# Kernel optimization log

Measured on AMD Instinct MI355X. Metric: run time of the kernel, lower is better.

## Reference

```python
import jax, jax.numpy as jnp
import numpy as np

ORDER = 2  # gcn_order (max diffusion step)


def _diffusion_conv(x, supports, W, b):
    """DCRNN diffusion graph conv.
    x: (B, C, N); supports: list of (N, N); W: (C*(len(supports)*ORDER+1), O); b: (O,)
    Chebyshev-style recurrence x_k = 2*A@x_{k-1} - x_{k-2}, as in original DCRNN.
    """
    feats = [x]
    for A in supports:
        x0 = x
        x1 = jnp.einsum('bcn,mn->bcm', x0, A)
        feats.append(x1)
        for _ in range(2, ORDER + 1):
            x2 = 2.0 * jnp.einsum('bcn,mn->bcm', x1, A) - x0
            feats.append(x2)
            x0, x1 = x1, x2
    h = jnp.concatenate(feats, axis=1)  # (B, C*num_matrices, N)
    return jnp.einsum('bcn,co->bon', h, W) + b[None, :, None]


def setup_inputs() -> dict:
    key = jax.random.key(0)
    ks = jax.random.split(key, 8)
    B, IN_DIM, HID, N = 64, 2, 64, 2048
    NUM_MAT = 2 * ORDER + 1  # num_supports*order + 1
    CIN = IN_DIM + HID  # 66
    inputs = jax.random.normal(ks[0], (B, IN_DIM, N), dtype=jnp.float32)
    hx = jax.random.normal(ks[1], (B, HID, N), dtype=jnp.float32)
    # random-walk style supports: nonnegative, row-normalized
    a0 = jax.random.uniform(ks[2], (N, N), dtype=jnp.float32)
    a1 = jax.random.uniform(ks[3], (N, N), dtype=jnp.float32)
    support0 = a0 / jnp.sum(a0, axis=1, keepdims=True)
    support1 = a1 / jnp.sum(a1, axis=1, keepdims=True)
    scale = 1.0 / np.sqrt(CIN * NUM_MAT)
    W_ru = jax.random.normal(ks[4], (CIN * NUM_MAT, 2 * HID), dtype=jnp.float32) * scale
    b_ru = jnp.ones((2 * HID,), dtype=jnp.float32)  # bias_start = 1.0
    W_c = jax.random.normal(ks[5], (CIN * NUM_MAT, HID), dtype=jnp.float32) * scale
    b_c = jnp.zeros((HID,), dtype=jnp.float32)
    return {"inputs": inputs, "hx": hx, "support0": support0, "support1": support1,
            "W_ru": W_ru, "b_ru": b_ru, "W_c": W_c, "b_c": b_c}


def reference(inputs, hx, support0, support1, W_ru, b_ru, W_c, b_c):
    supports = [support0, support1]
    hid = hx.shape[1]
    concat_input = jnp.concatenate([inputs, hx], axis=1)  # (B, in+hid, N)
    value = jax.nn.sigmoid(_diffusion_conv(concat_input, supports, W_ru, b_ru))
    r = value[:, :hid, :]
    u = value[:, hid:, :]
    C = jnp.tanh(_diffusion_conv(jnp.concatenate([inputs, r * hx], axis=1), supports, W_c, b_c))
    new_state = u * hx + (1.0 - u) * C
    return new_state
```

## Files before the change

### kernel.cpp

```cpp
#include <hip/hip_runtime.h>
#include <stdint.h>


typedef unsigned short ushort_t;
typedef __attribute__((ext_vector_type(8))) __bf16 bf16x8;
typedef __attribute__((ext_vector_type(4))) float f32x4;
typedef __attribute__((ext_vector_type(16))) float f32x16;
typedef __attribute__((ext_vector_type(8))) int i32x8;

#define KP 352
#define MROWS 131072

__device__ __forceinline__ ushort_t f2bf(float f) {
  union { float f; uint32_t u; } v; v.f = f;
  uint32_t r = v.u + 0x7FFFu + ((v.u >> 16) & 1u);
  return (ushort_t)(r >> 16);
}
__device__ __forceinline__ float bf2f(ushort_t u) {
  union { uint32_t u; float f; } v; v.u = ((uint32_t)u) << 16;
  return v.f;
}

__device__ __forceinline__ void gl_lds16(const void* g, void* l) {
  __builtin_amdgcn_global_load_lds(
      (const __attribute__((address_space(1))) void*)g,
      (__attribute__((address_space(3))) void*)l, 16, 0, 0);
}


__global__ void k_cast_f8(const float* __restrict__ src, uint32_t* __restrict__ dst,
                          int n4, float scale) {
  for (int i = blockIdx.x * 256 + threadIdx.x; i < n4; i += gridDim.x * 256) {
    float4 v = ((const float4*)src)[i];
    int r = __builtin_amdgcn_cvt_pk_fp8_f32(v.x * scale, v.y * scale, 0, 0);
    r = __builtin_amdgcn_cvt_pk_fp8_f32(v.z * scale, v.w * scale, r, 1);
    dst[i] = (uint32_t)r;
  }
}

__global__ void k_build_X(const float* __restrict__ inputs, const float* __restrict__ hx,
                          ushort_t* __restrict__ Xbf, uint8_t* __restrict__ Xf8) {
  int r = blockIdx.x;
  int b = r / 66, c = r - b * 66;
  const float* src = (c < 2) ? (inputs + ((size_t)b * 2 + c) * 2048)
                             : (hx + ((size_t)b * 64 + (c - 2)) * 2048);
  ushort_t* d1 = Xbf + (size_t)r * 2048;
  uint8_t* d2 = Xf8 + (size_t)r * 2048;
  for (int n = threadIdx.x * 4; n < 2048; n += 256 * 4) {
    float4 v = *(const float4*)(src + n);
    ushort4 rr;
    rr.x = f2bf(v.x); rr.y = f2bf(v.y); rr.z = f2bf(v.z); rr.w = f2bf(v.w);
    *(ushort4*)(d1 + n) = rr;
    int r8 = __builtin_amdgcn_cvt_pk_fp8_f32(v.x, v.y, 0, 0);
    r8 = __builtin_amdgcn_cvt_pk_fp8_f32(v.z, v.w, r8, 1);
    *(uint32_t*)(d2 + n) = (uint32_t)r8;
  }
}

__global__ void k_pack_W(const float* __restrict__ Wru, const float* __restrict__ Wc,
                         ushort_t* __restrict__ Wtru, ushort_t* __restrict__ Wtc) {
  int o = blockIdx.x;
  const float* W = (o < 128) ? Wru : Wc;
  int O = (o < 128) ? 128 : 64;
  int oo = (o < 128) ? o : (o - 128);
  ushort_t* Wt = (o < 128) ? Wtru : Wtc;
  for (int k = threadIdx.x; k < KP; k += 256) {
    float v = (k < 330 && oo < O) ? W[(size_t)k * O + oo] : 0.f;
    Wt[(size_t)oo * KP + k] = f2bf(v);
  }
}

__global__ __launch_bounds__(256) void k_trans_slot0(const ushort_t* __restrict__ Xbf,
                                                     ushort_t* __restrict__ Ht) {
  __shared__ ushort_t t[66 * 136];
  const int tid = threadIdx.x;
  const int b = blockIdx.y;
  const int n0 = blockIdx.x * 128;
  for (int idx = tid; idx < 66 * 16; idx += 256) {
    int c = idx >> 4, seg = idx & 15;
    bf16x8 v = *(const bf16x8*)&Xbf[((size_t)b * 66 + c) * 2048 + n0 + seg * 8];
    *(bf16x8*)&t[c * 136 + seg * 8] = v;
  }
  __syncthreads();
  for (int idx = tid; idx < 128 * 33; idx += 256) {
    int nn = idx / 33, pc = idx - nn * 33;
    int c = pc * 2;
    uint32_t pk = (uint32_t)t[c * 136 + nn] | ((uint32_t)t[(c + 1) * 136 + nn] << 16);
    *(uint32_t*)&Ht[((size_t)b * 2048 + n0 + nn) * KP + c] = pk;
  }
}

template <int MODE>
__global__ __launch_bounds__(256, 4) void gemm_bt(
    const uint8_t* __restrict__ Aop, int lda,
    const uint8_t* __restrict__ Bop,
    const ushort_t* __restrict__ Xres,
    uint8_t* __restrict__ Y1f8,
    ushort_t* __restrict__ Ht) {
  __shared__ char smem[33280];
  ushort_t* smemU = (ushort_t*)smem;
  const int tid = threadIdx.x;
  const int l = tid & 63, w = tid >> 6;
  const int wr = w >> 1, wc = w & 1;
  const int rowL = l & 31;
  const int kh = l >> 5;
  const int m7 = (rowL >> 2) & 7;

  const int fid = blockIdx.y * 33 + blockIdx.x;
  const int xcd = fid & 7;
  const int idx = fid >> 3;
  const int nb = xcd * 4 + idx / 33;
  const int mb = idx % 33;
  const int r0 = mb * 128;
  const int m0 = nb * 128;
  const int g = m0 >> 11;
  if (MODE == 1) Aop += (size_t)g * 2048;

  const int SA = (MODE == 0) ? 0x7F7F7F7F : 0x7A7A7A7A;
  const int SB = 0x76767676;

  f32x16 acc[2][2];
#pragma unroll
  for (int mi = 0; mi < 2; ++mi)
#pragma unroll
    for (int ni = 0; ni < 2; ++ni)
#pragma unroll
      for (int q = 0; q < 16; ++q) acc[mi][ni][q] = 0.f;

  const int d = tid;
  const int srow = ((d >> 3) << 2) | (((d >> 1) ^ (d >> 4)) & 1) |
                   ((((d >> 2) ^ (d >> 5)) & 1) << 1);
  const int sj = (d ^ (d >> 3)) & 1;
  const uint8_t* pA = Aop + (size_t)(r0 + srow) * lda + sj * 16;
  const uint8_t* pB = Bop + (size_t)(m0 + srow) * 2048 + sj * 16;

  const int sj0 = ((rowL * 2) ^ m7) * 16;
  const int sj1 = ((rowL * 2 + 1) ^ m7) * 16;
  const int aw = wr * 2048;
  const int bw = wc * 2048;

  const int kt0 = (idx & 3) * 4;
  for (int ktt = 0; ktt < 16; ++ktt) {
    const int kt = (ktt + kt0) & 15;
    const int kb = kt * 128;
#pragma unroll
    for (int kq = 0; kq < 4; ++kq) {
      gl_lds16(pA + kb + kq * 32, smem + kq * 4096 + tid * 16);
      gl_lds16(pB + kb + kq * 32, smem + 16384 + kq * 4096 + tid * 16);
    }
    __syncthreads();
#pragma unroll
    for (int kw = 0; kw < 2; ++kw) {
      const int rbase = (2 * kw + kh) * 4096;
      union { uint4 q[2]; i32x8 v; } bu[2], au;
#pragma unroll
      for (int ni = 0; ni < 2; ++ni) {
        const char* bp = smem + 16384 + rbase + bw + ni * 1024;
        bu[ni].q[0] = *(const uint4*)(bp + sj0);
        bu[ni].q[1] = *(const uint4*)(bp + sj1);
      }
#pragma unroll
      for (int mi = 0; mi < 2; ++mi) {
        const char* ap = smem + rbase + aw + mi * 1024;
        au.q[0] = *(const uint4*)(ap + sj0);
        au.q[1] = *(const uint4*)(ap + sj1);
#pragma unroll
        for (int ni = 0; ni < 2; ++ni)
          acc[mi][ni] = __builtin_amdgcn_mfma_scale_f32_32x32x64_f8f6f4(
              au.v, bu[ni].v, acc[mi][ni], 0, 0, 0, SA, 0, SB);
      }
    }
    __syncthreads();
  }

#pragma unroll
  for (int mi = 0; mi < 2; ++mi) {
#pragma unroll
    for (int ni = 0; ni < 2; ++ni) {
      const int clb = wc * 64 + ni * 32 + rowL;
#pragma unroll
      for (int q = 0; q < 16; ++q) {
        const int rl = wr * 64 + mi * 32 + (q & 3) + 8 * (q >> 2) + 4 * kh;
        float v = acc[mi][ni][q];
        if (MODE == 1)
          v = 2.f * v - bf2f(Xres[(size_t)(r0 + rl) * 2048 + ((m0 + clb) & 2047)]);
        smemU[clb * 130 + rl] = f2bf(v);
      }
    }
  }
  __syncthreads();

  const int slotBase = (MODE == 0 ? 1 : 2) + 2 * g;
  const int n_base = m0 & 2047;
#pragma unroll 4
  for (int j2 = 0; j2 < 32; ++j2) {
    int idx2 = j2 * 256 + tid;
    int mc = idx2 >> 6, pr = idx2 & 63;
    int rl = pr * 2;
    unsigned rg = (unsigned)(r0 + rl);
    unsigned b = rg / 66u;
    unsigned c = rg - b * 66u;
    int n = n_base + mc;
    uint32_t pk = (uint32_t)smemU[mc * 130 + rl] |
                  ((uint32_t)smemU[mc * 130 + rl + 1] << 16);
    *(uint32_t*)&Ht[((size_t)b * 2048 + n) * KP + slotBase * 66 + c] = pk;
  }

  if (MODE == 0) {
#pragma unroll 4
    for (int it = 0; it < 16; ++it) {
      int idx2 = it * 256 + tid;
      int rl = idx2 >> 5, mq = idx2 & 31;
      float v0 = bf2f(smemU[(mq * 4 + 0) * 130 + rl]) * 32.f;
      float v1 = bf2f(smemU[(mq * 4 + 1) * 130 + rl]) * 32.f;
      float v2 = bf2f(smemU[(mq * 4 + 2) * 130 + rl]) * 32.f;
      float v3 = bf2f(smemU[(mq * 4 + 3) * 130 + rl]) * 32.f;
      int r8 = __builtin_amdgcn_cvt_pk_fp8_f32(v0, v1, 0, 0);
      r8 = __builtin_amdgcn_cvt_pk_fp8_f32(v2, v3, r8, 1);
      *(uint32_t*)(Y1f8 + (size_t)(r0 + rl) * 4096 + m0 + mq * 4) = (uint32_t)r8;
    }
  }
}

template <int MODE>
__global__ __launch_bounds__(256, 4) void proj_mfma(
    const ushort_t* __restrict__ Ht_c, const ushort_t* __restrict__ Wt,
    const float* __restrict__ bias, const float* __restrict__ hx,
    ushort_t* __restrict__ Xbf, uint8_t* __restrict__ Xf8,
    ushort_t* __restrict__ Ubuf, ushort_t* __restrict__ HtW,
    float* __restrict__ out) {
  __shared__ ushort_t smem[16640];
  const int tid = threadIdx.x;
  const int l = tid & 63, w = tid >> 6;
  const int wr = w >> 1, wc = w & 1;
  const int lr = l & 15, lk = l >> 4;
  const int bb = blockIdx.x >> 4;
  const int n0 = (blockIdx.x & 15) * 128;
  const size_t m0 = (size_t)bb * 2048 + n0;

  f32x4 acc[4][4];
  const f32x4 zero = {0.f, 0.f, 0.f, 0.f};
#pragma unroll
  for (int mi = 0; mi < 4; mi++)
#pragma unroll
    for (int ni = 0; ni < 4; ni++) acc[mi][ni] = zero;

  const int srow = tid >> 2;
  const int kcol = ((tid & 3) ^ ((tid >> 3) & 3)) * 8;
  const ushort_t* pA = Ht_c + (m0 + srow) * KP + kcol;
  const ushort_t* pB = Wt + (size_t)srow * KP + kcol;
  const int so = (lk ^ ((lr >> 1) & 3)) * 8;

#define STAGEP(KT, BB)                                                         \
  {                                                                            \
    const int kp_ = (KT) * 32;                                                 \
    gl_lds16(pA + kp_, (void*)&smem[(BB) + tid * 8]);                          \
    gl_lds16(pA + (size_t)64 * KP + kp_, (void*)&smem[(BB) + 2048 + tid * 8]); \
    gl_lds16(pB + kp_, (void*)&smem[(BB) + 4096 + tid * 8]);                   \
    gl_lds16(pB + (size_t)64 * KP + kp_, (void*)&smem[(BB) + 6144 + tid * 8]); \
  }

#define COMPUTEP(BB)                                                           \
  {                                                                            \
    bf16x8 af[4], bfv[4];                                                      \
    _Pragma("unroll")                                                          \
    for (int i = 0; i < 4; i++)                                                \
      af[i] = *(const bf16x8*)&smem[(BB) + (wr * 64 + i * 16 + lr) * 32 + so]; \
    _Pragma("unroll")                                                          \
    for (int i = 0; i < 4; i++)                                                \
      bfv[i] = *(const bf16x8*)&smem[(BB) + 4096 + (wc * 64 + i * 16 + lr) * 32 + so]; \
    _Pragma("unroll")                                                          \
    for (int mi = 0; mi < 4; mi++)                                             \
      _Pragma("unroll")                                                        \
      for (int ni = 0; ni < 4; ni++)                                           \
        acc[mi][ni] = __builtin_amdgcn_mfma_f32_16x16x32_bf16(af[mi], bfv[ni], \
                                                              acc[mi][ni], 0, 0, 0); \
  }

  STAGEP(0, 0);
  __syncthreads();
#pragma unroll 1
  for (int kt = 0; kt < 11; ++kt) {
    if (kt + 1 < 11) STAGEP(kt + 1, ((kt + 1) & 1) * 8192);
    COMPUTEP((kt & 1) * 8192);
    __syncthreads();
  }

#undef STAGEP
#undef COMPUTEP

#pragma unroll
  for (int mi = 0; mi < 4; mi++) {
#pragma unroll
    for (int ni = 0; ni < 4; ni++) {
      const int rl0 = wr * 64 + mi * 16 + lk * 4;
      const int o = wc * 64 + ni * 16 + lr;
      float bv = (MODE == 0 || o < 64) ? bias[o] : 0.f;
#pragma unroll
      for (int j = 0; j < 4; j++) {
        float v = acc[mi][ni][j] + bv;
        float s;
        if (MODE == 0) s = 1.f / (1.f + expf(-v));
        else           s = tanhf(v);
        smem[o * 130 + rl0 + j] = f2bf(s);
      }
    }
  }
  __syncthreads();

  if (MODE == 0) {
#pragma unroll 4
    for (int j2 = 0; j2 < 64; ++j2) {
      int idx = j2 * 256 + tid;
      int o = idx >> 7, m = idx & 127;
      ushort_t sv = smem[o * 130 + m];
      if (o < 64) {
        float p = bf2f(sv) * hx[((size_t)bb * 64 + o) * 2048 + n0 + m];
        smem[o * 130 + m] = f2bf(p);
      } else {
        Ubuf[((size_t)bb * 64 + (o - 64)) * 2048 + n0 + m] = sv;
      }
    }
    __syncthreads();
#pragma unroll 2
    for (int j2 = 0; j2 < 8; ++j2) {
      int idx = j2 * 256 + tid;
      int o = idx >> 5, m4 = (idx & 31) * 4;
      ushort_t s0 = smem[o * 130 + m4 + 0], s1 = smem[o * 130 + m4 + 1];
      ushort_t s2 = smem[o * 130 + m4 + 2], s3 = smem[o * 130 + m4 + 3];
      ushort4 pk4; pk4.x = s0; pk4.y = s1; pk4.z = s2; pk4.w = s3;
      *(ushort4*)&Xbf[((size_t)bb * 66 + 2 + o) * 2048 + n0 + m4] = pk4;
      int r8 = __builtin_amdgcn_cvt_pk_fp8_f32(bf2f(s0), bf2f(s1), 0, 0);
      r8 = __builtin_amdgcn_cvt_pk_fp8_f32(bf2f(s2), bf2f(s3), r8, 1);
      *(uint32_t*)(Xf8 + ((size_t)bb * 66 + 2 + o) * 2048 + n0 + m4) = (uint32_t)r8;
    }
#pragma unroll 2
    for (int j2 = 0; j2 < 16; ++j2) {
      int idx = j2 * 256 + tid;
      int m = idx >> 5, po = idx & 31;
      int o = po * 2;
      uint32_t pk = (uint32_t)smem[o * 130 + m] |
                    ((uint32_t)smem[(o + 1) * 130 + m] << 16);
      *(uint32_t*)&HtW[((size_t)bb * 2048 + n0 + m) * KP + 2 + o] = pk;
    }
  } else {
#pragma unroll 4
    for (int j2 = 0; j2 < 32; ++j2) {
      int idx = j2 * 256 + tid;
      int o = idx >> 7, m = idx & 127;
      float Cv = bf2f(smem[o * 130 + m]);
      int n = n0 + m;
      size_t oi = ((size_t)bb * 64 + o) * 2048 + n;
      float u = bf2f(Ubuf[oi]);
      out[oi] = u * hx[oi] + (1.f - u) * Cv;
    }
  }
}


extern "C" void kernel_launch(void* const* d_in, const int* in_sizes, int n_in,
                              void* d_out, int out_size, void* d_ws, size_t ws_size,
                              hipStream_t stream) {
  (void)in_sizes; (void)n_in; (void)out_size; (void)ws_size;
  const float* inputs = (const float*)d_in[0];
  const float* hx     = (const float*)d_in[1];
  const float* s0     = (const float*)d_in[2];
  const float* s1     = (const float*)d_in[3];
  const float* W_ru   = (const float*)d_in[4];
  const float* b_ru   = (const float*)d_in[5];
  const float* W_c    = (const float*)d_in[6];
  const float* b_c    = (const float*)d_in[7];
  float* out = (float*)d_out;

  char* p = (char*)d_ws;
  uint8_t*  Abf8 = (uint8_t*)p;  p += (size_t)4096 * 2048;
  ushort_t* Xbf  = (ushort_t*)p; p += (size_t)4224 * 2048 * 2;
  uint8_t*  Xf8  = (uint8_t*)p;  p += (size_t)4224 * 2048;
  uint8_t*  Y1f8 = (uint8_t*)p;  p += (size_t)4224 * 4096;
  ushort_t* Ht   = (ushort_t*)p; p += (size_t)MROWS * KP * 2;
  ushort_t* Ubuf = (ushort_t*)p; p += (size_t)64 * 64 * 2048 * 2;
  ushort_t* Wtru = (ushort_t*)p; p += (size_t)128 * KP * 2;
  ushort_t* Wtc  = (ushort_t*)p; p += (size_t)128 * KP * 2;

  k_cast_f8<<<1024, 256, 0, stream>>>(s0, (uint32_t*)Abf8, 1048576, 512.f);
  k_cast_f8<<<1024, 256, 0, stream>>>(s1, (uint32_t*)(Abf8 + 4194304), 1048576, 512.f);
  k_build_X<<<4224, 256, 0, stream>>>(inputs, hx, Xbf, Xf8);
  k_pack_W<<<192, 256, 0, stream>>>(W_ru, W_c, Wtru, Wtc);

  dim3 g(33, 32);
  dim3 gt(16, 64);
  k_trans_slot0<<<gt, 256, 0, stream>>>(Xbf, Ht);
  gemm_bt<0><<<g, 256, 0, stream>>>(Xf8, 2048, Abf8, nullptr, Y1f8, Ht);
  gemm_bt<1><<<g, 256, 0, stream>>>(Y1f8, 4096, Abf8, Xbf, nullptr, Ht);
  proj_mfma<0><<<1024, 256, 0, stream>>>(Ht, Wtru, b_ru, hx, Xbf, Xf8, Ubuf, Ht, nullptr);
  gemm_bt<0><<<g, 256, 0, stream>>>(Xf8, 2048, Abf8, nullptr, Y1f8, Ht);
  gemm_bt<1><<<g, 256, 0, stream>>>(Y1f8, 4096, Abf8, Xbf, nullptr, Ht);
  proj_mfma<1><<<1024, 256, 0, stream>>>(Ht, Wtc, b_c, hx, nullptr, nullptr, Ubuf, nullptr, out);
}
```

Baseline: 446.6 us.

## Drop bf16 X buffer, swap GEMM operand roles for direct Ht epilogue writes

The separate bf16 copy of the concatenated input is removed. The slot-0 transpose now reads fp32 inputs/hx directly, and the MODE 1 residual is read from the slot-0 columns already stored in Ht. The GEMM swaps operand roles so each lane's accumulator columns map to one (b,c) row, and it writes bf16 results straight into Ht without an LDS transpose. LDS staging is kept only for the fp8 Y1 output, now with an XOR swizzle. This cuts a full bf16 buffer's writes and reads and one LDS round trip. The trade-off is scattered 2-byte global stores into Ht with a KP stride, which may coalesce poorly.

```diff
diff --git a/kernel.cpp b/kernel.cpp
--- a/kernel.cpp
+++ b/kernel.cpp
@@ -38,19 +38,15 @@
   }
 }
 
-__global__ void k_build_X(const float* __restrict__ inputs, const float* __restrict__ hx,
-                          ushort_t* __restrict__ Xbf, uint8_t* __restrict__ Xf8) {
+__global__ void k_build_Xf8(const float* __restrict__ inputs, const float* __restrict__ hx,
+                            uint8_t* __restrict__ Xf8) {
   int r = blockIdx.x;
   int b = r / 66, c = r - b * 66;
   const float* src = (c < 2) ? (inputs + ((size_t)b * 2 + c) * 2048)
                              : (hx + ((size_t)b * 64 + (c - 2)) * 2048);
-  ushort_t* d1 = Xbf + (size_t)r * 2048;
   uint8_t* d2 = Xf8 + (size_t)r * 2048;
   for (int n = threadIdx.x * 4; n < 2048; n += 256 * 4) {
     float4 v = *(const float4*)(src + n);
-    ushort4 rr;
-    rr.x = f2bf(v.x); rr.y = f2bf(v.y); rr.z = f2bf(v.z); rr.w = f2bf(v.w);
-    *(ushort4*)(d1 + n) = rr;
     int r8 = __builtin_amdgcn_cvt_pk_fp8_f32(v.x, v.y, 0, 0);
     r8 = __builtin_amdgcn_cvt_pk_fp8_f32(v.z, v.w, r8, 1);
     *(uint32_t*)(d2 + n) = (uint32_t)r8;
@@ -70,7 +66,8 @@
   }
 }
 
-__global__ __launch_bounds__(256) void k_trans_slot0(const ushort_t* __restrict__ Xbf,
+__global__ __launch_bounds__(256) void k_trans_slot0(const float* __restrict__ inputs,
+                                                     const float* __restrict__ hx,
                                                      ushort_t* __restrict__ Ht) {
   __shared__ ushort_t t[66 * 136];
   const int tid = threadIdx.x;
@@ -78,8 +75,13 @@
   const int n0 = blockIdx.x * 128;
   for (int idx = tid; idx < 66 * 16; idx += 256) {
     int c = idx >> 4, seg = idx & 15;
-    bf16x8 v = *(const bf16x8*)&Xbf[((size_t)b * 66 + c) * 2048 + n0 + seg * 8];
-    *(bf16x8*)&t[c * 136 + seg * 8] = v;
+    const float* src = (c < 2) ? (inputs + ((size_t)b * 2 + c) * 2048)
+                               : (hx + ((size_t)b * 64 + (c - 2)) * 2048);
+    float4 v0 = *(const float4*)(src + n0 + seg * 8);
+    float4 v1 = *(const float4*)(src + n0 + seg * 8 + 4);
+    ushort_t* dp = &t[c * 136 + seg * 8];
+    dp[0] = f2bf(v0.x); dp[1] = f2bf(v0.y); dp[2] = f2bf(v0.z); dp[3] = f2bf(v0.w);
+    dp[4] = f2bf(v1.x); dp[5] = f2bf(v1.y); dp[6] = f2bf(v1.z); dp[7] = f2bf(v1.w);
   }
   __syncthreads();
   for (int idx = tid; idx < 128 * 33; idx += 256) {
@@ -92,13 +94,11 @@
 
 template <int MODE>
 __global__ __launch_bounds__(256, 4) void gemm_bt(
-    const uint8_t* __restrict__ Aop, int lda,
-    const uint8_t* __restrict__ Bop,
-    const ushort_t* __restrict__ Xres,
+    const uint8_t* __restrict__ Xop, int ldx,
+    const uint8_t* __restrict__ Sop,
     uint8_t* __restrict__ Y1f8,
     ushort_t* __restrict__ Ht) {
-  __shared__ char smem[33280];
-  ushort_t* smemU = (ushort_t*)smem;
+  __shared__ char smem[32768];
   const int tid = threadIdx.x;
   const int l = tid & 63, w = tid >> 6;
   const int wr = w >> 1, wc = w & 1;
@@ -109,15 +109,15 @@
   const int fid = blockIdx.y * 33 + blockIdx.x;
   const int xcd = fid & 7;
   const int idx = fid >> 3;
-  const int nb = xcd * 4 + idx / 33;
-  const int mb = idx % 33;
-  const int r0 = mb * 128;
-  const int m0 = nb * 128;
+  const int mb = xcd * 4 + idx / 33;
+  const int rb = idx % 33;
+  const int m0 = mb * 128;
+  const int r0 = rb * 128;
   const int g = m0 >> 11;
-  if (MODE == 1) Aop += (size_t)g * 2048;
-
-  const int SA = (MODE == 0) ? 0x7F7F7F7F : 0x7A7A7A7A;
-  const int SB = 0x76767676;
+  if (MODE == 1) Xop += (size_t)g * 2048;
+
+  const int SS = 0x76767676;
+  const int SX = (MODE == 0) ? 0x7F7F7F7F : 0x7A7A7A7A;
 
   f32x16 acc[2][2];
 #pragma unroll
@@ -131,13 +131,13 @@
   const int srow = ((d >> 3) << 2) | (((d >> 1) ^ (d >> 4)) & 1) |
                    ((((d >> 2) ^ (d >> 5)) & 1) << 1);
   const int sj = (d ^ (d >> 3)) & 1;
-  const uint8_t* pA = Aop + (size_t)(r0 + srow) * lda + sj * 16;
-  const uint8_t* pB = Bop + (size_t)(m0 + srow) * 2048 + sj * 16;
+  const uint8_t* pX = Xop + (size_t)(r0 + srow) * ldx + sj * 16;
+  const uint8_t* pS = Sop + (size_t)(m0 + srow) * 2048 + sj * 16;
 
   const int sj0 = ((rowL * 2) ^ m7) * 16;
   const int sj1 = ((rowL * 2 + 1) ^ m7) * 16;
-  const int aw = wr * 2048;
-  const int bw = wc * 2048;
+  const int sw = wr * 2048;
+  const int xw = wc * 2048;
 
   const int kt0 = (idx & 3) * 4;
   for (int ktt = 0; ktt < 16; ++ktt) {
@@ -145,79 +145,75 @@
     const int kb = kt * 128;
 #pragma unroll
     for (int kq = 0; kq < 4; ++kq) {
-      gl_lds16(pA + kb + kq * 32, smem + kq * 4096 + tid * 16);
-      gl_lds16(pB + kb + kq * 32, smem + 16384 + kq * 4096 + tid * 16);
+      gl_lds16(pX + kb + kq * 32, smem + kq * 4096 + tid * 16);
+      gl_lds16(pS + kb + kq * 32, smem + 16384 + kq * 4096 + tid * 16);
     }
     __syncthreads();
 #pragma unroll
     for (int kw = 0; kw < 2; ++kw) {
       const int rbase = (2 * kw + kh) * 4096;
-      union { uint4 q[2]; i32x8 v; } bu[2], au;
+      union { uint4 q[2]; i32x8 v; } xu[2], su;
 #pragma unroll
       for (int ni = 0; ni < 2; ++ni) {
-        const char* bp = smem + 16384 + rbase + bw + ni * 1024;
-        bu[ni].q[0] = *(const uint4*)(bp + sj0);
-        bu[ni].q[1] = *(const uint4*)(bp + sj1);
+        const char* xp = smem + rbase + xw + ni * 1024;
+        xu[ni].q[0] = *(const uint4*)(xp + sj0);
+        xu[ni].q[1] = *(const uint4*)(xp + sj1);
       }
 #pragma unroll
       for (int mi = 0; mi < 2; ++mi) {
-        const char* ap = smem + rbase + aw + mi * 1024;
-        au.q[0] = *(const uint4*)(ap + sj0);
-        au.q[1] = *(const uint4*)(ap + sj1);
+        const char* sp = smem + 16384 + rbase + sw + mi * 1024;
+        su.q[0] = *(const uint4*)(sp + sj0);
+        su.q[1] = *(const uint4*)(sp + sj1);
 #pragma unroll
         for (int ni = 0; ni < 2; ++ni)
           acc[mi][ni] = __builtin_amdgcn_mfma_scale_f32_32x32x64_f8f6f4(
-              au.v, bu[ni].v, acc[mi][ni], 0, 0, 0, SA, 0, SB);
-      }
-    }
-    __syncthreads();
-  }
-
-#pragma unroll
-  for (int mi = 0; mi < 2; ++mi) {
-#pragma unroll
-    for (int ni = 0; ni < 2; ++ni) {
-      const int clb = wc * 64 + ni * 32 + rowL;
+              su.v, xu[ni].v, acc[mi][ni], 0, 0, 0, SS, 0, SX);
+      }
+    }
+    __syncthreads();
+  }
+
+  const int slotBase = (MODE == 0 ? 1 : 2) + 2 * g;
+  const int nb0 = m0 & 2047;
+  ushort_t* ldsY = (ushort_t*)smem;
+
+#pragma unroll
+  for (int ni = 0; ni < 2; ++ni) {
+    const int rcol = wc * 64 + ni * 32 + rowL;
+    const unsigned rg = (unsigned)(r0 + rcol);
+    const unsigned b = rg / 66u;
+    const unsigned c = rg - b * 66u;
+    const size_t hrow = (size_t)b * 2048;
+#pragma unroll
+    for (int mi = 0; mi < 2; ++mi) {
 #pragma unroll
       for (int q = 0; q < 16; ++q) {
-        const int rl = wr * 64 + mi * 32 + (q & 3) + 8 * (q >> 2) + 4 * kh;
+        const int mrow = wr * 64 + mi * 32 + (q & 3) + 8 * (q >> 2) + 4 * kh;
         float v = acc[mi][ni][q];
-        if (MODE == 1)
-          v = 2.f * v - bf2f(Xres[(size_t)(r0 + rl) * 2048 + ((m0 + clb) & 2047)]);
-        smemU[clb * 130 + rl] = f2bf(v);
-      }
-    }
-  }
-  __syncthreads();
-
-  const int slotBase = (MODE == 0 ? 1 : 2) + 2 * g;
-  const int n_base = m0 & 2047;
-#pragma unroll 4
-  for (int j2 = 0; j2 < 32; ++j2) {
-    int idx2 = j2 * 256 + tid;
-    int mc = idx2 >> 6, pr = idx2 & 63;
-    int rl = pr * 2;
-    unsigned rg = (unsigned)(r0 + rl);
-    unsigned b = rg / 66u;
-    unsigned c = rg - b * 66u;
-    int n = n_base + mc;
-    uint32_t pk = (uint32_t)smemU[mc * 130 + rl] |
-                  ((uint32_t)smemU[mc * 130 + rl + 1] << 16);
-    *(uint32_t*)&Ht[((size_t)b * 2048 + n) * KP + slotBase * 66 + c] = pk;
+        const size_t hbase = (hrow + nb0 + mrow) * KP;
+        if (MODE == 1) v = 2.f * v - bf2f(Ht[hbase + c]);
+        Ht[hbase + slotBase * 66 + c] = f2bf(v);
+        if (MODE == 0)
+          ldsY[mrow * 128 + (rcol ^ ((mrow << 1) & 127))] = f2bf(v);
+      }
+    }
   }
 
   if (MODE == 0) {
+    __syncthreads();
 #pragma unroll 4
     for (int it = 0; it < 16; ++it) {
       int idx2 = it * 256 + tid;
-      int rl = idx2 >> 5, mq = idx2 & 31;
-      float v0 = bf2f(smemU[(mq * 4 + 0) * 130 + rl]) * 32.f;
-      float v1 = bf2f(smemU[(mq * 4 + 1) * 130 + rl]) * 32.f;
-      float v2 = bf2f(smemU[(mq * 4 + 2) * 130 + rl]) * 32.f;
-      float v3 = bf2f(smemU[(mq * 4 + 3) * 130 + rl]) * 32.f;
-      int r8 = __builtin_amdgcn_cvt_pk_fp8_f32(v0, v1, 0, 0);
-      r8 = __builtin_amdgcn_cvt_pk_fp8_f32(v2, v3, r8, 1);
-      *(uint32_t*)(Y1f8 + (size_t)(r0 + rl) * 4096 + m0 + mq * 4) = (uint32_t)r8;
+      int r = idx2 >> 5, md = idx2 & 31;
+      float vv[4];
+#pragma unroll
+      for (int j = 0; j < 4; ++j) {
+        int m = md * 4 + j;
+        vv[j] = bf2f(ldsY[m * 128 + (r ^ ((m << 1) & 127))]) * 32.f;
+      }
+      int r8 = __builtin_amdgcn_cvt_pk_fp8_f32(vv[0], vv[1], 0, 0);
+      r8 = __builtin_amdgcn_cvt_pk_fp8_f32(vv[2], vv[3], r8, 1);
+      *(uint32_t*)(Y1f8 + (size_t)(r0 + r) * 4096 + m0 + md * 4) = (uint32_t)r8;
     }
   }
 }
@@ -226,9 +222,8 @@
 __global__ __launch_bounds__(256, 4) void proj_mfma(
     const ushort_t* __restrict__ Ht_c, const ushort_t* __restrict__ Wt,
     const float* __restrict__ bias, const float* __restrict__ hx,
-    ushort_t* __restrict__ Xbf, uint8_t* __restrict__ Xf8,
-    ushort_t* __restrict__ Ubuf, ushort_t* __restrict__ HtW,
-    float* __restrict__ out) {
+    uint8_t* __restrict__ Xf8, ushort_t* __restrict__ Ubuf,
+    ushort_t* __restrict__ HtW, float* __restrict__ out) {
   __shared__ ushort_t smem[16640];
   const int tid = threadIdx.x;
   const int l = tid & 63, w = tid >> 6;
@@ -326,12 +321,10 @@
     for (int j2 = 0; j2 < 8; ++j2) {
       int idx = j2 * 256 + tid;
       int o = idx >> 5, m4 = (idx & 31) * 4;
-      ushort_t s0 = smem[o * 130 + m4 + 0], s1 = smem[o * 130 + m4 + 1];
-      ushort_t s2 = smem[o * 130 + m4 + 2], s3 = smem[o * 130 + m4 + 3];
-      ushort4 pk4; pk4.x = s0; pk4.y = s1; pk4.z = s2; pk4.w = s3;
-      *(ushort4*)&Xbf[((size_t)bb * 66 + 2 + o) * 2048 + n0 + m4] = pk4;
-      int r8 = __builtin_amdgcn_cvt_pk_fp8_f32(bf2f(s0), bf2f(s1), 0, 0);
-      r8 = __builtin_amdgcn_cvt_pk_fp8_f32(bf2f(s2), bf2f(s3), r8, 1);
+      float p0 = bf2f(smem[o * 130 + m4 + 0]), p1 = bf2f(smem[o * 130 + m4 + 1]);
+      float p2 = bf2f(smem[o * 130 + m4 + 2]), p3 = bf2f(smem[o * 130 + m4 + 3]);
+      int r8 = __builtin_amdgcn_cvt_pk_fp8_f32(p0, p1, 0, 0);
+      r8 = __builtin_amdgcn_cvt_pk_fp8_f32(p2, p3, r8, 1);
       *(uint32_t*)(Xf8 + ((size_t)bb * 66 + 2 + o) * 2048 + n0 + m4) = (uint32_t)r8;
     }
 #pragma unroll 2
@@ -374,7 +367,6 @@
 
   char* p = (char*)d_ws;
   uint8_t*  Abf8 = (uint8_t*)p;  p += (size_t)4096 * 2048;
-  ushort_t* Xbf  = (ushort_t*)p; p += (size_t)4224 * 2048 * 2;
   uint8_t*  Xf8  = (uint8_t*)p;  p += (size_t)4224 * 2048;
   uint8_t*  Y1f8 = (uint8_t*)p;  p += (size_t)4224 * 4096;
   ushort_t* Ht   = (ushort_t*)p; p += (size_t)MROWS * KP * 2;
@@ -384,16 +376,16 @@
 
   k_cast_f8<<<1024, 256, 0, stream>>>(s0, (uint32_t*)Abf8, 1048576, 512.f);
   k_cast_f8<<<1024, 256, 0, stream>>>(s1, (uint32_t*)(Abf8 + 4194304), 1048576, 512.f);
-  k_build_X<<<4224, 256, 0, stream>>>(inputs, hx, Xbf, Xf8);
+  k_build_Xf8<<<4224, 256, 0, stream>>>(inputs, hx, Xf8);
   k_pack_W<<<192, 256, 0, stream>>>(W_ru, W_c, Wtru, Wtc);
 
   dim3 g(33, 32);
   dim3 gt(16, 64);
-  k_trans_slot0<<<gt, 256, 0, stream>>>(Xbf, Ht);
-  gemm_bt<0><<<g, 256, 0, stream>>>(Xf8, 2048, Abf8, nullptr, Y1f8, Ht);
-  gemm_bt<1><<<g, 256, 0, stream>>>(Y1f8, 4096, Abf8, Xbf, nullptr, Ht);
-  proj_mfma<0><<<1024, 256, 0, stream>>>(Ht, Wtru, b_ru, hx, Xbf, Xf8, Ubuf, Ht, nullptr);
-  gemm_bt<0><<<g, 256, 0, stream>>>(Xf8, 2048, Abf8, nullptr, Y1f8, Ht);
-  gemm_bt<1><<<g, 256, 0, stream>>>(Y1f8, 4096, Abf8, Xbf, nullptr, Ht);
-  proj_mfma<1><<<1024, 256, 0, stream>>>(Ht, Wtc, b_c, hx, nullptr, nullptr, Ubuf, nullptr, out);
-}
+  k_trans_slot0<<<gt, 256, 0, stream>>>(inputs, hx, Ht);
+  gemm_bt<0><<<g, 256, 0, stream>>>(Xf8, 2048, Abf8, Y1f8, Ht);
+  gemm_bt<1><<<g, 256, 0, stream>>>(Y1f8, 4096, Abf8, nullptr, Ht);
+  proj_mfma<0><<<1024, 256, 0, stream>>>(Ht, Wtru, b_ru, hx, Xf8, Ubuf, Ht, nullptr);
+  gemm_bt<0><<<g, 256, 0, stream>>>(Xf8, 2048, Abf8, Y1f8, Ht);
+  gemm_bt<1><<<g, 256, 0, stream>>>(Y1f8, 4096, Abf8, nullptr, Ht);
+  proj_mfma<1><<<1024, 256, 0, stream>>>(Ht, Wtc, b_c, hx, nullptr, Ubuf, nullptr, out);
+}
```

Result: slower. 540.6 us (+21.0%).

## Double-buffer FP8 MFMA K-loop with async LDS prefetch of next tile

Applied to the files above, without the earlier changes.

Splits the K loop into 32 smaller steps and ping-pongs between two 16KB LDS buffers. The next tile's global-to-LDS loads are issued before computing on the current one, with explicit vmcnt waits and raw barriers. This is meant to overlap global memory latency with MFMA work instead of stalling at each sync. Each step now does half the MFMAs, so there are more barriers per unit of work, and correctness depends on the vmcnt count matching the number of outstanding loads.

```diff
diff --git a/kernel.cpp b/kernel.cpp
--- a/kernel.cpp
+++ b/kernel.cpp
@@ -139,39 +139,56 @@
   const int aw = wr * 2048;
   const int bw = wc * 2048;
 
-  const int kt0 = (idx & 3) * 4;
-  for (int ktt = 0; ktt < 16; ++ktt) {
-    const int kt = (ktt + kt0) & 15;
-    const int kb = kt * 128;
-#pragma unroll
-    for (int kq = 0; kq < 4; ++kq) {
-      gl_lds16(pA + kb + kq * 32, smem + kq * 4096 + tid * 16);
-      gl_lds16(pB + kb + kq * 32, smem + 16384 + kq * 4096 + tid * 16);
-    }
-    __syncthreads();
-#pragma unroll
-    for (int kw = 0; kw < 2; ++kw) {
-      const int rbase = (2 * kw + kh) * 4096;
-      union { uint4 q[2]; i32x8 v; } bu[2], au;
-#pragma unroll
-      for (int ni = 0; ni < 2; ++ni) {
-        const char* bp = smem + 16384 + rbase + bw + ni * 1024;
-        bu[ni].q[0] = *(const uint4*)(bp + sj0);
-        bu[ni].q[1] = *(const uint4*)(bp + sj1);
-      }
-#pragma unroll
-      for (int mi = 0; mi < 2; ++mi) {
-        const char* ap = smem + rbase + aw + mi * 1024;
-        au.q[0] = *(const uint4*)(ap + sj0);
-        au.q[1] = *(const uint4*)(ap + sj1);
-#pragma unroll
-        for (int ni = 0; ni < 2; ++ni)
-          acc[mi][ni] = __builtin_amdgcn_mfma_scale_f32_32x32x64_f8f6f4(
-              au.v, bu[ni].v, acc[mi][ni], 0, 0, 0, SA, 0, SB);
-      }
-    }
-    __syncthreads();
-  }
+#define STAGEF(TT, BB)                                                       \
+  {                                                                          \
+    const int kb_ = (TT) * 64;                                               \
+    gl_lds16(pA + kb_,      smem + (BB) + tid * 16);                         \
+    gl_lds16(pA + kb_ + 32, smem + (BB) + 4096 + tid * 16);                  \
+    gl_lds16(pB + kb_,      smem + (BB) + 8192 + tid * 16);                  \
+    gl_lds16(pB + kb_ + 32, smem + (BB) + 8192 + 4096 + tid * 16);           \
+  }
+
+#define COMPUTEF(BB)                                                         \
+  {                                                                          \
+    const int rbase = kh * 4096;                                             \
+    union { uint4 q[2]; i32x8 v; } bu[2], au;                                \
+    _Pragma("unroll")                                                        \
+    for (int ni = 0; ni < 2; ++ni) {                                         \
+      const char* bp = smem + (BB) + 8192 + rbase + bw + ni * 1024;          \
+      bu[ni].q[0] = *(const uint4*)(bp + sj0);                               \
+      bu[ni].q[1] = *(const uint4*)(bp + sj1);                               \
+    }                                                                        \
+    _Pragma("unroll")                                                        \
+    for (int mi = 0; mi < 2; ++mi) {                                         \
+      const char* ap = smem + (BB) + rbase + aw + mi * 1024;                 \
+      au.q[0] = *(const uint4*)(ap + sj0);                                   \
+      au.q[1] = *(const uint4*)(ap + sj1);                                   \
+      _Pragma("unroll")                                                      \
+      for (int ni = 0; ni < 2; ++ni)                                         \
+        acc[mi][ni] = __builtin_amdgcn_mfma_scale_f32_32x32x64_f8f6f4(       \
+            au.v, bu[ni].v, acc[mi][ni], 0, 0, 0, SA, 0, SB);                \
+    }                                                                        \
+  }
+
+  const int kt0 = (idx & 3) * 8;
+  STAGEF(kt0, 0);
+#pragma unroll 1
+  for (int ktt = 0; ktt < 32; ++ktt) {
+    const int cur = (ktt & 1) * 16384;
+    if (ktt + 1 < 32) {
+      STAGEF(((ktt + 1 + kt0) & 31), cur ^ 16384);
+      asm volatile("s_waitcnt vmcnt(4)" ::: "memory");
+    } else {
+      asm volatile("s_waitcnt vmcnt(0)" ::: "memory");
+    }
+    __builtin_amdgcn_s_barrier();
+    __builtin_amdgcn_sched_barrier(0);
+    COMPUTEF(cur);
+    __builtin_amdgcn_s_barrier();
+  }
+
+#undef STAGEF
+#undef COMPUTEF
 
 #pragma unroll
   for (int mi = 0; mi < 2; ++mi) {
```

Result: faster. 414.4 us (-7.2%).
